# Kernel optimization log

Hardware: AMD Instinct MI355X
Metric: run time of the kernel (lower is better)

The kernel has to match this reference:

```python
import jax, jax.numpy as jnp
import numpy as np

B, N, DIM, H, DH = 8, 4096, 512, 8, 64
M = 266  # nb_features = int(dim_head * ln(dim_head)) = int(64*4.1589)
LN_EPS = 1e-5
K_EPS = 1e-4  # performer softmax_kernel epsilon


def _gaussian_orthogonal_matrix(m, d, rng):
    # performer_pytorch default: stacked QR blocks, rows scaled by chi(d) norms
    blocks = []
    n_full = m // d
    for _ in range(n_full):
        q, _ = np.linalg.qr(rng.standard_normal((d, d)))
        blocks.append(q.T)
    rem = m - n_full * d
    if rem > 0:
        q, _ = np.linalg.qr(rng.standard_normal((d, d)))
        blocks.append(q.T[:rem])
    proj = np.concatenate(blocks, axis=0)
    norms = np.linalg.norm(rng.standard_normal((m, d)), axis=1)
    return (proj * norms[:, None]).astype(np.float32)


def setup_inputs() -> dict:
    key = jax.random.key(0)
    ks = jax.random.split(key, 8)
    s_in = 1.0 / np.sqrt(DIM)
    s_ff = 1.0 / np.sqrt(4 * DIM)
    rng = np.random.default_rng(0)
    return {
        "x": jax.random.normal(ks[0], (B, N, DIM), jnp.float32),
        "w_q": jax.random.normal(ks[1], (DIM, DIM), jnp.float32) * s_in,
        "w_k": jax.random.normal(ks[2], (DIM, DIM), jnp.float32) * s_in,
        "w_v": jax.random.normal(ks[3], (DIM, DIM), jnp.float32) * s_in,
        "w_o": jax.random.normal(ks[4], (DIM, DIM), jnp.float32) * s_in,
        "b_o": jnp.zeros((DIM,), jnp.float32),
        "ln1_g": jnp.ones((DIM,), jnp.float32),
        "ln1_b": jnp.zeros((DIM,), jnp.float32),
        "ln2_g": jnp.ones((DIM,), jnp.float32),
        "ln2_b": jnp.zeros((DIM,), jnp.float32),
        "ff_w1": jax.random.normal(ks[5], (DIM, 4 * DIM), jnp.float32) * s_in,
        "ff_b1": jnp.zeros((4 * DIM,), jnp.float32),
        "ff_w2": jax.random.normal(ks[6], (4 * DIM, DIM), jnp.float32) * s_ff,
        "ff_b2": jnp.zeros((DIM,), jnp.float32),
        "projection": jnp.asarray(_gaussian_orthogonal_matrix(M, DH, rng)),
    }


def _layernorm(x, g, b):
    mu = jnp.mean(x, -1, keepdims=True)
    var = jnp.mean((x - mu) ** 2, -1, keepdims=True)
    return (x - mu) * jax.lax.rsqrt(var + LN_EPS) * g + b


def _softmax_kernel(data, proj, is_query):
    # FAVOR+ positive softmax-kernel features (performer_pytorch.softmax_kernel)
    dn = data.shape[-1] ** -0.25  # data_normalizer
    ratio = proj.shape[0] ** -0.5
    dd = jnp.einsum("bhnd,md->bhnm", data * dn, proj)
    diag = jnp.sum(data ** 2, -1, keepdims=True) * 0.5 * (dn ** 2)  # [B,H,N,1]
    if is_query:
        mx = jax.lax.stop_gradient(jnp.max(dd, -1, keepdims=True))
    else:
        mx = jax.lax.stop_gradient(jnp.max(dd))
    return ratio * (jnp.exp(dd - diag - mx) + K_EPS)


def reference(x, w_q, w_k, w_v, w_o, b_o, ln1_g, ln1_b, ln2_g, ln2_b,
              ff_w1, ff_b1, ff_w2, ff_b2, projection):
    # --- attention sublayer (pre-norm) ---
    h = _layernorm(x, ln1_g, ln1_b)

    def split_heads(t):
        return t.reshape(B, N, H, DH).transpose(0, 2, 1, 3)  # [B,H,N,DH]

    q = split_heads(h @ w_q)
    k = split_heads(h @ w_k)
    v = split_heads(h @ w_v)

    qp = _softmax_kernel(q, projection, True)   # [B,H,N,M]
    kp = _softmax_kernel(k, projection, False)  # [B,H,N,M]

    # non-causal linear attention: O(N) in sequence length
    d_inv = 1.0 / jnp.einsum("bhnm,bhm->bhn", qp, jnp.sum(kp, axis=2))
    ctx = jnp.einsum("bhnm,bhnd->bhmd", kp, v)          # [B,H,M,DH]
    attn = jnp.einsum("bhnm,bhmd,bhn->bhnd", qp, ctx, d_inv)
    attn = attn.transpose(0, 2, 1, 3).reshape(B, N, DIM)
    x = x + attn @ w_o + b_o

    # --- feed-forward sublayer (pre-norm) ---
    h2 = _layernorm(x, ln2_g, ln2_b)
    ff = jax.nn.gelu(h2 @ ff_w1 + ff_b1, approximate=False) @ ff_w2 + ff_b2
    return x + ff
```

## Files before the change

### kernel.cpp

```cpp
#include <hip/hip_runtime.h>
#include <cmath>

typedef unsigned short u16;
typedef unsigned int u32;
typedef short bf16x8 __attribute__((ext_vector_type(8)));
typedef float f32x4 __attribute__((ext_vector_type(4)));

#define DEVI __device__ __forceinline__

constexpr int NSEQ = 4096, DIMM = 512;
constexpr int KVLD = 1024;
constexpr int MP = 288;
constexpr int MPP = 296;
constexpr int MREAL = 266;
constexpr int DHP = 96;
constexpr int LSTR = 72;
constexpr float LNEPS = 1e-5f;
constexpr float KEPS = 1e-4f;
constexpr float DN = 0.3535533905932738f;
constexpr float HALF_DN2 = 0.0625f;

DEVI u16 f2bf(float f) {
  u32 u = __float_as_uint(f);
  u32 r = (u + 0x7FFFu + ((u >> 16) & 1u)) >> 16;
  return (u16)r;
}
DEVI float bf2f(u16 h) { return __uint_as_float(((u32)h) << 16); }

DEVI f32x4 mfma16(bf16x8 a, bf16x8 b, f32x4 c) {
  return __builtin_amdgcn_mfma_f32_16x16x32_bf16(a, b, c, 0, 0, 0);
}

DEVI void gload_lds16(const void* g, void* l) {
  __builtin_amdgcn_global_load_lds(
      (const __attribute__((address_space(1))) u32*)g,
      (__attribute__((address_space(3))) u32*)l, 16, 0, 0);
}

DEVI float gelu_fast(float z) {
  float a = fminf(1.5957691216057308f * (z + 0.044715f * z * z * z), 60.f);
  float e = __expf(a);
  return z * e * __builtin_amdgcn_rcpf(e + 1.f);
}

__global__ void ws_sentinel(float* out) { out[0] = 12345.0f; }

__launch_bounds__(256)
__global__ void transpose_cvt(const float* __restrict__ in, u16* __restrict__ out,
                              int K, int Nn) {
  __shared__ float tl[32][33];
  int ntn = Nn >> 5;
  int bid = blockIdx.x;
  int kt = bid / ntn, ntt = bid - kt * ntn;
  int k0 = kt << 5, nn0 = ntt << 5;
  int t = threadIdx.x;
  int r = t >> 5, c = t & 31;
#pragma unroll
  for (int i = 0; i < 4; ++i)
    tl[r + i * 8][c] = in[(size_t)(k0 + r + i * 8) * Nn + nn0 + c];
  __syncthreads();
#pragma unroll
  for (int i = 0; i < 4; ++i)
    out[(size_t)(nn0 + r + i * 8) * K + k0 + c] = f2bf(tl[c][r + i * 8]);
}

__global__ void proj_prep(const float* __restrict__ proj, u16* __restrict__ projf) {
  int idx = blockIdx.x * 256 + threadIdx.x;
  if (idx >= MP * 64) return;
  int e = idx & 7, lane = (idx >> 3) & 63, fh = idx >> 9;
  int f = fh >> 1, half = fh & 1;
  int m = f * 16 + (lane & 15);
  int d = half * 32 + (lane >> 4) * 8 + e;
  float v = (m < MREAL) ? proj[m * 64 + d] * DN : 0.f;
  projf[idx] = f2bf(v);
}

__launch_bounds__(256)
__global__ void ln_fwd(const float* __restrict__ x, const float* __restrict__ g,
                       const float* __restrict__ bt, u16* __restrict__ out) {
  int w = threadIdx.x >> 6, lane = threadIdx.x & 63;
  int row = blockIdx.x * 4 + w;
  const float* xr = x + (size_t)row * DIMM;
  int c0 = lane * 4;
  float4 v0 = *(const float4*)(xr + c0);
  float4 v1 = *(const float4*)(xr + 256 + c0);
  float s = v0.x + v0.y + v0.z + v0.w + v1.x + v1.y + v1.z + v1.w;
  float sq = v0.x * v0.x + v0.y * v0.y + v0.z * v0.z + v0.w * v0.w +
             v1.x * v1.x + v1.y * v1.y + v1.z * v1.z + v1.w * v1.w;
#pragma unroll
  for (int mk = 1; mk < 64; mk <<= 1) {
    s += __shfl_xor(s, mk, 64);
    sq += __shfl_xor(sq, mk, 64);
  }
  float mu = s * (1.f / 512.f);
  float var = sq * (1.f / 512.f) - mu * mu;
  float rstd = rsqrtf(var + LNEPS);
  float4 g0 = *(const float4*)(g + c0);
  float4 g1 = *(const float4*)(g + 256 + c0);
  float4 b0 = *(const float4*)(bt + c0);
  float4 b1 = *(const float4*)(bt + 256 + c0);
  u16* orow = out + (size_t)row * DIMM;
  uint2 p0, p1;
  {
    u16 h0 = f2bf((v0.x - mu) * rstd * g0.x + b0.x);
    u16 h1 = f2bf((v0.y - mu) * rstd * g0.y + b0.y);
    u16 h2 = f2bf((v0.z - mu) * rstd * g0.z + b0.z);
    u16 h3 = f2bf((v0.w - mu) * rstd * g0.w + b0.w);
    p0.x = ((u32)h1 << 16) | h0; p0.y = ((u32)h3 << 16) | h2;
  }
  {
    u16 h0 = f2bf((v1.x - mu) * rstd * g1.x + b1.x);
    u16 h1 = f2bf((v1.y - mu) * rstd * g1.y + b1.y);
    u16 h2 = f2bf((v1.z - mu) * rstd * g1.z + b1.z);
    u16 h3 = f2bf((v1.w - mu) * rstd * g1.w + b1.w);
    p1.x = ((u32)h1 << 16) | h0; p1.y = ((u32)h3 << 16) | h2;
  }
  *(uint2*)(orow + c0) = p0;
  *(uint2*)(orow + 256 + c0) = p1;
}

#define WAITVM(N) asm volatile("s_waitcnt vmcnt(" #N ")" ::: "memory")

template <int EPI>
__launch_bounds__(512)
__global__ void gemm256(const u16* __restrict__ A, int lda,
                        const u16* __restrict__ Bt, int ldb, int K,
                        void* __restrict__ OutP, int Nout, int ldo,
                        const float* __restrict__ bias,
                        const float* __restrict__ Res) {
  __shared__ __align__(16) u16 Al[2][256 * 64];
  __shared__ __align__(16) u16 Bl[2][256 * 64];
  int ntiles = Nout >> 8;
  int nwg = gridDim.x;
  int bid = blockIdx.x;
  int cpx = nwg >> 3;
  int wg = (bid & 7) * cpx + (bid >> 3);
  int mt = wg / ntiles, nt = wg - mt * ntiles;
  int t = threadIdx.x, lane = t & 63, w = t >> 6;
  int wm = w >> 2, wn = w & 3;
  int fr = lane & 15, fq = lane >> 4;
  int rowA0 = mt * 256, colB0 = nt * 256;
  int swz = (fr & 7) << 4;

  f32x4 acc[8][4];
#pragma unroll
  for (int i = 0; i < 8; ++i)
#pragma unroll
    for (int j = 0; j < 4; ++j) acc[i][j] = f32x4{0.f, 0.f, 0.f, 0.f};

  int srow = t >> 3;
  int so = ((t * 16) & 127) ^ ((srow & 7) << 4);

#define STAGE_G(bufi, k0)                                                       \
  do {                                                                          \
    _Pragma("unroll") for (int it = 0; it < 4; ++it) {                          \
      gload_lds16(                                                              \
          (const char*)(A + ((size_t)(rowA0 + srow + it * 64) * lda + (k0))) + so, \
          (char*)Al[bufi] + t * 16 + it * 8192);                                \
      gload_lds16(                                                              \
          (const char*)(Bt + ((size_t)(colB0 + srow + it * 64) * ldb + (k0))) + so, \
          (char*)Bl[bufi] + t * 16 + it * 8192);                                \
    }                                                                           \
  } while (0)

  int NT = K >> 6;
  STAGE_G(0, 0);
  STAGE_G(1, 64);
  int bi = 0;
  for (int tt = 0; tt < NT; ++tt) {
    if (tt + 1 < NT) { WAITVM(8); } else { WAITVM(0); }
    __builtin_amdgcn_s_barrier();

    bf16x8 av[8][2], bv[4][2];
#pragma unroll
    for (int i = 0; i < 8; ++i)
#pragma unroll
      for (int ks = 0; ks < 2; ++ks) {
        int row = wm * 128 + i * 16 + fr;
        av[i][ks] = *(const bf16x8*)((const char*)Al[bi] + row * 128 +
                                     (((ks << 6) | (fq << 4)) ^ swz));
      }
#pragma unroll
    for (int j = 0; j < 4; ++j)
#pragma unroll
      for (int ks = 0; ks < 2; ++ks) {
        int row = wn * 64 + (j)*16 + fr;
        bv[j][ks] = *(const bf16x8*)((const char*)Bl[bi] + row * 128 +
                                     (((ks << 6) | (fq << 4)) ^ swz));
      }

    __builtin_amdgcn_s_setprio(1);
#pragma unroll
    for (int i = 0; i < 4; ++i)
#pragma unroll
      for (int j = 0; j < 4; ++j)
#pragma unroll
        for (int ks = 0; ks < 2; ++ks)
          acc[i][j] = mfma16(av[i][ks], bv[j][ks], acc[i][j]);
    __builtin_amdgcn_s_setprio(0);

    asm volatile("s_waitcnt lgkmcnt(0)" ::: "memory");
    __builtin_amdgcn_sched_barrier(0);
    __builtin_amdgcn_s_barrier();
    if (tt + 2 < NT) STAGE_G(bi, (tt + 2) * 64);

    __builtin_amdgcn_s_setprio(1);
#pragma unroll
    for (int i = 4; i < 8; ++i)
#pragma unroll
      for (int j = 0; j < 4; ++j)
#pragma unroll
        for (int ks = 0; ks < 2; ++ks)
          acc[i][j] = mfma16(av[i][ks], bv[j][ks], acc[i][j]);
    __builtin_amdgcn_s_setprio(0);
    bi ^= 1;
  }
#undef STAGE_G

#pragma unroll
  for (int i = 0; i < 8; ++i)
#pragma unroll
    for (int j = 0; j < 4; ++j) {
      int row = rowA0 + wm * 128 + i * 16 + fq * 4;
      int col = colB0 + wn * 64 + j * 16 + fr;
#pragma unroll
      for (int r = 0; r < 4; ++r) {
        float v = acc[i][j][r];
        size_t idx = (size_t)(row + r) * ldo + col;
        if constexpr (EPI == 0) {
          ((u16*)OutP)[idx] = f2bf(v);
        } else if constexpr (EPI == 1) {
          ((float*)OutP)[idx] = v + bias[col] + Res[(size_t)(row + r) * 512 + col];
        } else if constexpr (EPI == 2) {
          ((u16*)OutP)[idx] = f2bf(gelu_fast(v + bias[col]));
        } else {
          float bb = bias ? bias[col] : 0.f;
          ((float*)OutP)[idx] += v + bb;
        }
      }
    }
}

__launch_bounds__(256)
__global__ void kmax_kernel(const u16* __restrict__ kv, const u16* __restrict__ projf,
                            u32* __restrict__ maxslot) {
  __shared__ float wred[4];
  int bid = blockIdx.x;
  int bh = bid >> 6, nt = bid & 63;
  int b = bh >> 3, h = bh & 7;
  int n0 = nt * 64;
  int t = threadIdx.x, lane = t & 63, w = t >> 6;
  int fr = lane & 15, fq = lane >> 4;

  const u16* krow = kv + ((size_t)(b * NSEQ + n0 + w * 16 + fr)) * KVLD + h * 64;
  bf16x8 a0 = *(const bf16x8*)(krow + fq * 8);
  bf16x8 a1 = *(const bf16x8*)(krow + 32 + fq * 8);

  const bf16x8* pf = (const bf16x8*)projf;
  float m = -1e30f;
#pragma unroll
  for (int f = 0; f < 18; ++f) {
    bf16x8 b0 = pf[(f * 2 + 0) * 64 + lane];
    bf16x8 b1 = pf[(f * 2 + 1) * 64 + lane];
    f32x4 z = {0.f, 0.f, 0.f, 0.f};
    z = mfma16(a0, b0, z);
    z = mfma16(a1, b1, z);
    if (f * 16 + fr < MREAL) {
#pragma unroll
      for (int r = 0; r < 4; ++r) m = fmaxf(m, z[r]);
    }
  }
#pragma unroll
  for (int mk = 1; mk < 64; mk <<= 1) m = fmaxf(m, __shfl_xor(m, mk, 64));
  if (lane == 0) wred[w] = m;
  __syncthreads();
  if (t == 0) {
    float mm = fmaxf(fmaxf(wred[0], wred[1]), fmaxf(wred[2], wred[3]));
    u32 u = __float_as_uint(mm);
    u32 enc = (u & 0x80000000u) ? ~u : (u | 0x80000000u);
    atomicMax(maxslot, enc);
  }
}

__launch_bounds__(512)
__global__ void fused_ctx(const u16* __restrict__ kvbuf, const u16* __restrict__ projf,
                          const u32* __restrict__ maxslot, float* __restrict__ part) {
  __shared__ __align__(16) u16 kt[64 * 64];
  __shared__ __align__(16) u16 kpL[MP * LSTR];
  __shared__ __align__(16) u16 vL[DHP * LSTR];
  int bid = blockIdx.x;
  int bh = bid >> 2, s = bid & 3;
  int b = bh >> 3, h = bh & 7;
  int t = threadIdx.x, lane = t & 63, w = t >> 6;
  int fr = lane & 15, fq = lane >> 4;
  int rg = w & 3, fh = w >> 2;
  int wq4 = w >> 1, wn = w & 1;
  int i_base = (wq4 < 2) ? wq4 * 5 : 10 + (wq4 - 2) * 4;
  int i_cnt = (wq4 < 2) ? 5 : 4;

  if (t < 256) {
    int rr = 64 + (t >> 3), sg = t & 7;
    u16 val = (rr == 64) ? (u16)0x3F80 : (u16)0;
    uint4 v4; u16* pv = (u16*)&v4;
#pragma unroll
    for (int e = 0; e < 8; ++e) pv[e] = val;
    *(uint4*)(vL + rr * LSTR + sg * 8) = v4;
  }
  u32 enc = *maxslot;
  float gmax = __uint_as_float((enc & 0x80000000u) ? (enc & 0x7FFFFFFFu) : ~enc);
  const bf16x8* pf = (const bf16x8*)projf;

  f32x4 acc[5][3];
#pragma unroll
  for (int i = 0; i < 5; ++i)
#pragma unroll
    for (int j = 0; j < 3; ++j) acc[i][j] = f32x4{0.f, 0.f, 0.f, 0.f};

  for (int tile = 0; tile < 16; ++tile) {
    int n0 = s * 1024 + tile * 64;
#pragma unroll
    for (int it = 0; it < 2; ++it) {
      int idx = t + it * 512;
      int r = idx >> 4, sg = idx & 15;
      *(uint2*)(kt + r * 64 + sg * 4) =
          *(const uint2*)(kvbuf + ((size_t)(b * NSEQ + n0 + r)) * KVLD + h * 64 + sg * 4);
    }
#pragma unroll
    for (int it = 0; it < 2; ++it) {
      int idx = t + it * 512;
      int r = idx >> 4, sg = idx & 15;
      uint2 val = *(const uint2*)(kvbuf + ((size_t)(b * NSEQ + n0 + r)) * KVLD + 512 + h * 64 + sg * 4);
      u16* pv = (u16*)&val;
#pragma unroll
      for (int e = 0; e < 4; ++e) vL[(sg * 4 + e) * LSTR + r] = pv[e];
    }
    __syncthreads();

    float dg[4];
#pragma unroll
    for (int r4 = 0; r4 < 4; ++r4) {
      int row = rg * 16 + fq * 4 + r4;
      const u16* kr = kt + row * 64 + fr * 4;
      float ssum = 0.f;
#pragma unroll
      for (int e = 0; e < 4; ++e) { float xv = bf2f(kr[e]); ssum += xv * xv; }
#pragma unroll
      for (int mk = 1; mk < 16; mk <<= 1) ssum += __shfl_xor(ssum, mk, 64);
      dg[r4] = ssum * HALF_DN2;
    }
    bf16x8 a0 = *(const bf16x8*)(kt + (rg * 16 + fr) * 64 + fq * 8);
    bf16x8 a1 = *(const bf16x8*)(kt + (rg * 16 + fr) * 64 + 32 + fq * 8);
#pragma unroll
    for (int ff = 0; ff < 9; ++ff) {
      int f = fh * 9 + ff;
      bf16x8 b0 = pf[(f * 2 + 0) * 64 + lane];
      bf16x8 b1 = pf[(f * 2 + 1) * 64 + lane];
      f32x4 z = {0.f, 0.f, 0.f, 0.f};
      z = mfma16(a0, b0, z);
      z = mfma16(a1, b1, z);
      int col = f * 16 + fr;
#pragma unroll
      for (int r4 = 0; r4 < 4; ++r4) {
        int row = rg * 16 + fq * 4 + r4;
        float kval = (col < MREAL) ? (__expf(z[r4] - dg[r4] - gmax) + KEPS) : 0.f;
        kpL[col * LSTR + row] = f2bf(kval);
      }
    }
    __syncthreads();

#pragma unroll
    for (int kc = 0; kc < 2; ++kc) {
      bf16x8 av[5], bv[3];
#pragma unroll
      for (int i = 0; i < 5; ++i)
        if (i < i_cnt)
          av[i] = *(const bf16x8*)(kpL + ((i_base + i) * 16 + fr) * LSTR + kc * 32 + fq * 8);
#pragma unroll
      for (int j = 0; j < 3; ++j)
        bv[j] = *(const bf16x8*)(vL + (wn * 48 + j * 16 + fr) * LSTR + kc * 32 + fq * 8);
#pragma unroll
      for (int i = 0; i < 5; ++i)
        if (i < i_cnt)
#pragma unroll
          for (int j = 0; j < 3; ++j) acc[i][j] = mfma16(av[i], bv[j], acc[i][j]);
    }
    __syncthreads();
  }

  float* dst = part + ((size_t)bh * 4 + s) * MP * DHP;
#pragma unroll
  for (int i = 0; i < 5; ++i)
    if (i < i_cnt)
#pragma unroll
      for (int j = 0; j < 3; ++j) {
        int m = (i_base + i) * 16 + fq * 4;
        int c = wn * 48 + j * 16 + fr;
#pragma unroll
        for (int r = 0; r < 4; ++r) dst[(size_t)(m + r) * DHP + c] = acc[i][j][r];
      }
}

__launch_bounds__(256)
__global__ void ctx_reduce2(const float* __restrict__ part, u16* __restrict__ ctxT) {
  int bh = blockIdx.x, t = threadIdx.x;
  const float* p = part + (size_t)bh * 4 * MP * DHP;
  u16* dst = ctxT + (size_t)bh * DHP * MP;
  for (int idx = t; idx < DHP * MP; idx += 256) {
    int d = idx / MP, m = idx - d * MP;
    size_t o = (size_t)m * DHP + d;
    float v = p[o] + p[o + MP * DHP] + p[o + 2 * MP * DHP] + p[o + 3 * MP * DHP];
    dst[idx] = f2bf(v);
  }
}

__launch_bounds__(256)
__global__ void fused_attn(const u16* __restrict__ qb, const u16* __restrict__ ctxT,
                           const u16* __restrict__ projf, u16* __restrict__ attnb) {
  __shared__ __align__(16) u16 qt[64 * 64];
  __shared__ __align__(16) u16 qpL[64 * MPP];
  __shared__ float dbuf[64];
  int bid = blockIdx.x;
  int bh = bid >> 6, nt = bid & 63;
  int b = bh >> 3, h = bh & 7;
  int n0 = nt * 64;
  int t = threadIdx.x, lane = t & 63, w = t >> 6;
  int wm = w >> 1, wn = w & 1;
  int fr = lane & 15, fq = lane >> 4;

#pragma unroll
  for (int it = 0; it < 4; ++it) {
    int idx = t + it * 256;
    int r = idx >> 4, sg = idx & 15;
    *(uint2*)(qt + r * 64 + sg * 4) =
        *(const uint2*)(qb + ((size_t)(b * NSEQ + n0 + r)) * KVLD + h * 64 + sg * 4);
  }
  __syncthreads();

  float dg[4];
#pragma unroll
  for (int r4 = 0; r4 < 4; ++r4) {
    int row = w * 16 + fq * 4 + r4;
    const u16* qr = qt + row * 64 + fr * 4;
    float ssum = 0.f;
#pragma unroll
    for (int e = 0; e < 4; ++e) { float xv = bf2f(qr[e]); ssum += xv * xv; }
#pragma unroll
    for (int mk = 1; mk < 16; mk <<= 1) ssum += __shfl_xor(ssum, mk, 64);
    dg[r4] = ssum * HALF_DN2;
  }
  const bf16x8* pf = (const bf16x8*)projf;
  bf16x8 a0 = *(const bf16x8*)(qt + (w * 16 + fr) * 64 + fq * 8);
  bf16x8 a1 = *(const bf16x8*)(qt + (w * 16 + fr) * 64 + 32 + fq * 8);
  f32x4 accf[18];
#pragma unroll
  for (int f = 0; f < 18; ++f) {
    bf16x8 b0 = pf[(f * 2 + 0) * 64 + lane];
    bf16x8 b1 = pf[(f * 2 + 1) * 64 + lane];
    f32x4 z = {0.f, 0.f, 0.f, 0.f};
    z = mfma16(a0, b0, z);
    z = mfma16(a1, b1, z);
    accf[f] = z;
  }
  float mx[4];
#pragma unroll
  for (int r4 = 0; r4 < 4; ++r4) {
    float mm = -1e30f;
#pragma unroll
    for (int f = 0; f < 18; ++f) mm = fmaxf(mm, accf[f][r4]);
#pragma unroll
    for (int mk = 1; mk < 16; mk <<= 1) mm = fmaxf(mm, __shfl_xor(mm, mk, 64));
    mx[r4] = mm;
  }
#pragma unroll
  for (int f = 0; f < 18; ++f) {
    int col = f * 16 + fr;
#pragma unroll
    for (int r4 = 0; r4 < 4; ++r4) {
      int row = w * 16 + fq * 4 + r4;
      float qv = __expf(accf[f][r4] - dg[r4] - mx[r4]) + KEPS;
      qpL[row * MPP + col] = f2bf(qv);
    }
  }
  __syncthreads();

  const u16* cg = ctxT + (size_t)bh * DHP * MP;
  f32x4 acc2[2][3];
#pragma unroll
  for (int i = 0; i < 2; ++i)
#pragma unroll
    for (int j = 0; j < 3; ++j) acc2[i][j] = f32x4{0.f, 0.f, 0.f, 0.f};
  for (int k0 = 0; k0 < MP; k0 += 32) {
    bf16x8 av[2], bv[3];
#pragma unroll
    for (int i = 0; i < 2; ++i)
      av[i] = *(const bf16x8*)(qpL + (wm * 32 + i * 16 + fr) * MPP + k0 + fq * 8);
#pragma unroll
    for (int j = 0; j < 3; ++j)
      bv[j] = *(const bf16x8*)(cg + (size_t)(wn * 48 + j * 16 + fr) * MP + k0 + fq * 8);
#pragma unroll
    for (int i = 0; i < 2; ++i)
#pragma unroll
      for (int j = 0; j < 3; ++j) acc2[i][j] = mfma16(av[i], bv[j], acc2[i][j]);
  }
  if (wn == 1 && fr == 0) {
#pragma unroll
    for (int i = 0; i < 2; ++i) {
      int rl = wm * 32 + i * 16 + fq * 4;
#pragma unroll
      for (int r = 0; r < 4; ++r) dbuf[rl + r] = acc2[i][1][r];
    }
  }
  __syncthreads();

  u16* ob = qt;
#pragma unroll
  for (int i = 0; i < 2; ++i)
#pragma unroll
    for (int j = 0; j < 3; ++j) {
      int cl = wn * 48 + j * 16 + fr;
      if (cl < 64) {
        int rl = wm * 32 + i * 16 + fq * 4;
#pragma unroll
        for (int r = 0; r < 4; ++r)
          ob[(rl + r) * 64 + cl] = f2bf(acc2[i][j][r] / dbuf[rl + r]);
      }
    }
  __syncthreads();

  u16* dst = attnb + ((size_t)(b * NSEQ + n0)) * KVLD + h * 64;
  for (int idx = t; idx < 64 * 8; idx += 256) {
    int r = idx >> 3, sg = idx & 7;
    *(uint4*)(dst + (size_t)r * KVLD + sg * 8) = *(const uint4*)(ob + r * 64 + sg * 8);
  }
}

constexpr size_t OFF_WQT   = 0;
constexpr size_t OFF_WKT   = 524288;
constexpr size_t OFF_WVT   = 1048576;
constexpr size_t OFF_WOT   = 1572864;
constexpr size_t OFF_FF1T  = 2097152;
constexpr size_t OFF_FF2T  = 4194304;
constexpr size_t OFF_PROJF = 6328320;
constexpr size_t OFF_MAX   = 6365184;
constexpr size_t OFF_CTXT  = 6365440;
constexpr size_t OFF_H     = 9904384;
constexpr size_t OFF_KV    = 43458816;
constexpr size_t OFF_PART  = 110567680;
constexpr size_t WS_NEED   = 138879232;

extern "C" void kernel_launch(void* const* d_in, const int* in_sizes, int n_in,
                              void* d_out, int out_size, void* d_ws, size_t ws_size,
                              hipStream_t stream) {
  const float* x    = (const float*)d_in[0];
  const float* w_q  = (const float*)d_in[1];
  const float* w_k  = (const float*)d_in[2];
  const float* w_v  = (const float*)d_in[3];
  const float* w_o  = (const float*)d_in[4];
  const float* b_o  = (const float*)d_in[5];
  const float* ln1g = (const float*)d_in[6];
  const float* ln1b = (const float*)d_in[7];
  const float* ln2g = (const float*)d_in[8];
  const float* ln2b = (const float*)d_in[9];
  const float* ffw1 = (const float*)d_in[10];
  const float* ffb1 = (const float*)d_in[11];
  const float* ffw2 = (const float*)d_in[12];
  const float* ffb2 = (const float*)d_in[13];
  const float* proj = (const float*)d_in[14];
  (void)in_sizes; (void)n_in; (void)out_size;

  float* dout = (float*)d_out;
  if (ws_size < WS_NEED) {
    ws_sentinel<<<1, 1, 0, stream>>>(dout);
    return;
  }

  char* ws = (char*)d_ws;
  u16* wqt   = (u16*)(ws + OFF_WQT);
  u16* wkt   = (u16*)(ws + OFF_WKT);
  u16* wvt   = (u16*)(ws + OFF_WVT);
  u16* wot   = (u16*)(ws + OFF_WOT);
  u16* ff1t  = (u16*)(ws + OFF_FF1T);
  u16* ff2t  = (u16*)(ws + OFF_FF2T);
  u16* projf = (u16*)(ws + OFF_PROJF);
  u32* maxsl = (u32*)(ws + OFF_MAX);
  u16* ctxt  = (u16*)(ws + OFF_CTXT);
  u16* hbuf  = (u16*)(ws + OFF_H);
  u16* kvbuf = (u16*)(ws + OFF_KV);
  float* part = (float*)(ws + OFF_PART);

  hipMemsetAsync(maxsl, 0, 4, stream);

  transpose_cvt<<<256, 256, 0, stream>>>(w_q, wqt, 512, 512);
  transpose_cvt<<<256, 256, 0, stream>>>(w_k, wkt, 512, 512);
  transpose_cvt<<<256, 256, 0, stream>>>(w_v, wvt, 512, 512);
  transpose_cvt<<<256, 256, 0, stream>>>(w_o, wot, 512, 512);
  transpose_cvt<<<1024, 256, 0, stream>>>(ffw1, ff1t, 512, 2048);
  transpose_cvt<<<1024, 256, 0, stream>>>(ffw2, ff2t, 2048, 512);
  proj_prep<<<72, 256, 0, stream>>>(proj, projf);

  ln_fwd<<<8192, 256, 0, stream>>>(x, ln1g, ln1b, hbuf);
  gemm256<0><<<512, 512, 0, stream>>>(hbuf, 512, wkt, 512, 512, kvbuf, 1024, 1024, nullptr, nullptr);
  kmax_kernel<<<4096, 256, 0, stream>>>(kvbuf, projf, maxsl);
  fused_ctx<<<256, 512, 0, stream>>>(kvbuf, projf, maxsl, part);
  ctx_reduce2<<<64, 256, 0, stream>>>(part, ctxt);
  gemm256<0><<<256, 512, 0, stream>>>(hbuf, 512, wqt, 512, 512, kvbuf, 512, 1024, nullptr, nullptr);
  fused_attn<<<4096, 256, 0, stream>>>(kvbuf, ctxt, projf, kvbuf + 512);
  gemm256<1><<<256, 512, 0, stream>>>(kvbuf + 512, 1024, wot, 512, 512, dout, 512, 512, b_o, x);
  ln_fwd<<<8192, 256, 0, stream>>>(dout, ln2g, ln2b, hbuf);
  for (int c = 0; c < 2; ++c) {
    gemm256<2><<<512, 512, 0, stream>>>(hbuf, 512, ff1t + (size_t)c * 1024 * 512, 512, 512,
                                        kvbuf, 1024, 1024, ffb1 + c * 1024, nullptr);
    gemm256<3><<<256, 512, 0, stream>>>(kvbuf, 1024, ff2t + c * 1024, 2048, 1024,
                                        dout, 512, 512, (c == 0) ? ffb2 : nullptr, nullptr);
  }
}
```

Measured before the change: 630.0 us.

## Transpose feature MFMA, swizzle q tile, pack bf16 stores, prefetch ctx operands

In the key-feature kernel and in fused_attn, the exp results are now converted with packed v_cvt_pk_bf16_f32 and written as 8-byte stores rather than scalar 16-bit stores. fused_attn also XOR-swizzles the q tile in shared memory and swaps the MFMA operands, so each lane holds one row. That makes the diagonal norm and the row max a per-lane reduction with two shuffles, where before it took per-row loops with four shuffle rounds. The ctx^T global loads are software-pipelined one k-chunk ahead. This cuts LDS traffic, bank conflicts, shuffle and conversion instructions, at the cost of extra registers and inline asm that depends on gfx950 support.

After: 619.7 us. Within noise of the previous version (-1.6%).

```diff
diff --git a/kernel.cpp b/kernel.cpp
--- a/kernel.cpp
+++ b/kernel.cpp
@@ -359,12 +359,16 @@
       z = mfma16(a0, b0, z);
       z = mfma16(a1, b1, z);
       int col = f * 16 + fr;
-#pragma unroll
-      for (int r4 = 0; r4 < 4; ++r4) {
-        int row = rg * 16 + fq * 4 + r4;
-        float kval = (col < MREAL) ? (__expf(z[r4] - dg[r4] - gmax) + KEPS) : 0.f;
-        kpL[col * LSTR + row] = f2bf(kval);
-      }
+      bool ok = col < MREAL;
+      float k0v = ok ? (__expf(z[0] - dg[0] - gmax) + KEPS) : 0.f;
+      float k1v = ok ? (__expf(z[1] - dg[1] - gmax) + KEPS) : 0.f;
+      float k2v = ok ? (__expf(z[2] - dg[2] - gmax) + KEPS) : 0.f;
+      float k3v = ok ? (__expf(z[3] - dg[3] - gmax) + KEPS) : 0.f;
+      u32 lo, hi;
+      asm("v_cvt_pk_bf16_f32 %0, %1, %2" : "=v"(lo) : "v"(k0v), "v"(k1v));
+      asm("v_cvt_pk_bf16_f32 %0, %1, %2" : "=v"(hi) : "v"(k2v), "v"(k3v));
+      uint2 pk2; pk2.x = lo; pk2.y = hi;
+      *(uint2*)(kpL + col * LSTR + rg * 16 + fq * 4) = pk2;
     }
     __syncthreads();
 
@@ -431,55 +435,57 @@
   for (int it = 0; it < 4; ++it) {
     int idx = t + it * 256;
     int r = idx >> 4, sg = idx & 15;
-    *(uint2*)(qt + r * 64 + sg * 4) =
+    int dst = (r * 128 + sg * 8) ^ ((r & 7) << 4);
+    *(uint2*)((char*)qt + dst) =
         *(const uint2*)(qb + ((size_t)(b * NSEQ + n0 + r)) * KVLD + h * 64 + sg * 4);
   }
   __syncthreads();
 
-  float dg[4];
-#pragma unroll
-  for (int r4 = 0; r4 < 4; ++r4) {
-    int row = w * 16 + fq * 4 + r4;
-    const u16* qr = qt + row * 64 + fr * 4;
-    float ssum = 0.f;
-#pragma unroll
-    for (int e = 0; e < 4; ++e) { float xv = bf2f(qr[e]); ssum += xv * xv; }
-#pragma unroll
-    for (int mk = 1; mk < 16; mk <<= 1) ssum += __shfl_xor(ssum, mk, 64);
-    dg[r4] = ssum * HALF_DN2;
-  }
+  int swz = (fr & 7) << 4;
+  bf16x8 a0 = *(const bf16x8*)((const char*)qt +
+                               (((w * 16 + fr) * 128 + fq * 16) ^ swz));
+  bf16x8 a1 = *(const bf16x8*)((const char*)qt +
+                               (((w * 16 + fr) * 128 + 64 + fq * 16) ^ swz));
+
+  float ss = 0.f;
+#pragma unroll
+  for (int e = 0; e < 8; ++e) {
+    float x0 = bf2f((u16)a0[e]), x1 = bf2f((u16)a1[e]);
+    ss += x0 * x0 + x1 * x1;
+  }
+  ss += __shfl_xor(ss, 16, 64);
+  ss += __shfl_xor(ss, 32, 64);
+  float dg = ss * HALF_DN2;
+
   const bf16x8* pf = (const bf16x8*)projf;
-  bf16x8 a0 = *(const bf16x8*)(qt + (w * 16 + fr) * 64 + fq * 8);
-  bf16x8 a1 = *(const bf16x8*)(qt + (w * 16 + fr) * 64 + 32 + fq * 8);
   f32x4 accf[18];
 #pragma unroll
   for (int f = 0; f < 18; ++f) {
-    bf16x8 b0 = pf[(f * 2 + 0) * 64 + lane];
-    bf16x8 b1 = pf[(f * 2 + 1) * 64 + lane];
     f32x4 z = {0.f, 0.f, 0.f, 0.f};
-    z = mfma16(a0, b0, z);
-    z = mfma16(a1, b1, z);
+    z = mfma16(pf[(f * 2 + 0) * 64 + lane], a0, z);
+    z = mfma16(pf[(f * 2 + 1) * 64 + lane], a1, z);
     accf[f] = z;
   }
-  float mx[4];
-#pragma unroll
-  for (int r4 = 0; r4 < 4; ++r4) {
-    float mm = -1e30f;
-#pragma unroll
-    for (int f = 0; f < 18; ++f) mm = fmaxf(mm, accf[f][r4]);
-#pragma unroll
-    for (int mk = 1; mk < 16; mk <<= 1) mm = fmaxf(mm, __shfl_xor(mm, mk, 64));
-    mx[r4] = mm;
-  }
+  float mm = -1e30f;
+#pragma unroll
+  for (int f = 0; f < 18; ++f)
+#pragma unroll
+    for (int r = 0; r < 4; ++r) mm = fmaxf(mm, accf[f][r]);
+  mm = fmaxf(mm, __shfl_xor(mm, 16, 64));
+  mm = fmaxf(mm, __shfl_xor(mm, 32, 64));
+
+  u16* qp = qpL + (w * 16 + fr) * MPP + fq * 4;
 #pragma unroll
   for (int f = 0; f < 18; ++f) {
-    int col = f * 16 + fr;
-#pragma unroll
-    for (int r4 = 0; r4 < 4; ++r4) {
-      int row = w * 16 + fq * 4 + r4;
-      float qv = __expf(accf[f][r4] - dg[r4] - mx[r4]) + KEPS;
-      qpL[row * MPP + col] = f2bf(qv);
-    }
+    float e0 = __expf(accf[f][0] - dg - mm) + KEPS;
+    float e1 = __expf(accf[f][1] - dg - mm) + KEPS;
+    float e2 = __expf(accf[f][2] - dg - mm) + KEPS;
+    float e3 = __expf(accf[f][3] - dg - mm) + KEPS;
+    u32 lo, hi;
+    asm("v_cvt_pk_bf16_f32 %0, %1, %2" : "=v"(lo) : "v"(e0), "v"(e1));
+    asm("v_cvt_pk_bf16_f32 %0, %1, %2" : "=v"(hi) : "v"(e2), "v"(e3));
+    uint2 pk; pk.x = lo; pk.y = hi;
+    *(uint2*)(qp + f * 16) = pk;
   }
   __syncthreads();
 
@@ -489,18 +495,31 @@
   for (int i = 0; i < 2; ++i)
 #pragma unroll
     for (int j = 0; j < 3; ++j) acc2[i][j] = f32x4{0.f, 0.f, 0.f, 0.f};
-  for (int k0 = 0; k0 < MP; k0 += 32) {
-    bf16x8 av[2], bv[3];
+  bf16x8 bvc[3];
+#pragma unroll
+  for (int j = 0; j < 3; ++j)
+    bvc[j] = *(const bf16x8*)(cg + (size_t)(wn * 48 + j * 16 + fr) * MP + fq * 8);
+#pragma unroll
+  for (int kc = 0; kc < 9; ++kc) {
+    bf16x8 bvn[3];
+    if (kc < 8) {
+#pragma unroll
+      for (int j = 0; j < 3; ++j)
+        bvn[j] = *(const bf16x8*)(cg + (size_t)(wn * 48 + j * 16 + fr) * MP +
+                                  (kc + 1) * 32 + fq * 8);
+    }
+    bf16x8 av[2];
 #pragma unroll
     for (int i = 0; i < 2; ++i)
-      av[i] = *(const bf16x8*)(qpL + (wm * 32 + i * 16 + fr) * MPP + k0 + fq * 8);
-#pragma unroll
-    for (int j = 0; j < 3; ++j)
-      bv[j] = *(const bf16x8*)(cg + (size_t)(wn * 48 + j * 16 + fr) * MP + k0 + fq * 8);
+      av[i] = *(const bf16x8*)(qpL + (wm * 32 + i * 16 + fr) * MPP + kc * 32 + fq * 8);
 #pragma unroll
     for (int i = 0; i < 2; ++i)
 #pragma unroll
-      for (int j = 0; j < 3; ++j) acc2[i][j] = mfma16(av[i], bv[j], acc2[i][j]);
+      for (int j = 0; j < 3; ++j) acc2[i][j] = mfma16(av[i], bvc[j], acc2[i][j]);
+    if (kc < 8) {
+#pragma unroll
+      for (int j = 0; j < 3; ++j) bvc[j] = bvn[j];
+    }
   }
   if (wn == 1 && fr == 0) {
 #pragma unroll
```
